# Optimization experiments

Hardware: AMD Instinct MI355X
Metric: run time of the kernel (lower is better)

The kernel has to match this reference:

```python
import jax, jax.numpy as jnp
import numpy as np
import math

D_MODEL = 1024
N_HEADS = 16
D_HEAD = D_MODEL // N_HEADS


def setup_inputs() -> dict:
    key = jax.random.key(0)
    ks = jax.random.split(key, 9)
    B, S = 4, 2048
    scale = 1.0 / math.sqrt(D_MODEL)
    x = jax.random.normal(ks[0], (B, S, D_MODEL), dtype=jnp.float32)
    # nn.Linear weights stored as [out, in]; we keep [in, out] for x @ W
    w_q = jax.random.uniform(ks[1], (D_MODEL, D_MODEL), jnp.float32, -scale, scale)
    b_q = jax.random.uniform(ks[2], (D_MODEL,), jnp.float32, -scale, scale)
    w_k = jax.random.uniform(ks[3], (D_MODEL, D_MODEL), jnp.float32, -scale, scale)
    b_k = jax.random.uniform(ks[4], (D_MODEL,), jnp.float32, -scale, scale)
    w_v = jax.random.uniform(ks[5], (D_MODEL, D_MODEL), jnp.float32, -scale, scale)
    b_v = jax.random.uniform(ks[6], (D_MODEL,), jnp.float32, -scale, scale)
    w_o = jax.random.uniform(ks[7], (D_MODEL, D_MODEL), jnp.float32, -scale, scale)
    b_o = jax.random.uniform(ks[8], (D_MODEL,), jnp.float32, -scale, scale)
    return {"x": x, "w_q": w_q, "b_q": b_q, "w_k": w_k, "b_k": b_k,
            "w_v": w_v, "b_v": b_v, "w_o": w_o, "b_o": b_o}


def reference(x, w_q, b_q, w_k, b_k, w_v, b_v, w_o, b_o):
    B, S, _ = x.shape
    def split_heads(t):  # [B,S,D] -> [B,H,S,Dh]
        return t.reshape(B, S, N_HEADS, D_HEAD).transpose(0, 2, 1, 3)
    q = split_heads(x @ w_q + b_q)
    k = split_heads(x @ w_k + b_k)
    v = split_heads(x @ w_v + b_v)
    scores = jnp.einsum('bhqd,bhkd->bhqk', q, k) / math.sqrt(D_HEAD)
    attn = jax.nn.softmax(scores, axis=-1)  # dropout p=0 -> identity
    ctx = jnp.einsum('bhqk,bhkd->bhqd', attn, v)
    ctx = ctx.transpose(0, 2, 1, 3).reshape(B, S, D_MODEL)
    return ctx @ w_o + b_o
```

## Files before the change

kernel.cpp:

```cpp
#include <hip/hip_runtime.h>
#include <hip/hip_bf16.h>

#define DM   1024
#define SEQ  2048
#define NH   16
#define DH   64
#define BH   64
#define MTOT 8192

typedef __attribute__((ext_vector_type(8)))  short short8;
typedef __attribute__((ext_vector_type(4)))  short short4v;
typedef __attribute__((ext_vector_type(4)))  float f32x4;
typedef __attribute__((ext_vector_type(16))) float f32x16;
typedef __attribute__((ext_vector_type(4)))  float fvec4;
typedef __attribute__((ext_vector_type(4)))  int   i32x4;
typedef unsigned short ushort_t;

#define AS1 __attribute__((address_space(1)))
#define AS3 __attribute__((address_space(3)))

#define QSCALE 0.18033688011112042f
#define THR_L2 11.541560327111707f

static __device__ __forceinline__ unsigned short f2bf(float f){
  __bf16 h = (__bf16)f;
  return __builtin_bit_cast(unsigned short, h);
}

static __device__ __forceinline__ float fexp2(float x){
  float r;
  asm("v_exp_f32 %0, %1\n\ts_nop 0" : "=v"(r) : "v"(x));
  return r;
}

static __device__ __forceinline__ void gld16(const void* g, void* l){
  __builtin_amdgcn_global_load_lds((const AS1 int*)g, (AS3 int*)l, 16, 0, 0);
}

__global__ void k_cast_x(const float* __restrict__ x, ushort_t* __restrict__ xb){
  const size_t i = (size_t)blockIdx.x*256 + threadIdx.x;
  const fvec4* xv = (const fvec4*)x;
  fvec4 a = xv[2*i], b = xv[2*i+1];
  short8 r;
  #pragma unroll
  for (int j=0;j<4;++j) r[j]   = (short)f2bf(a[j]);
  #pragma unroll
  for (int j=0;j<4;++j) r[4+j] = (short)f2bf(b[j]);
  ((short8*)xb)[i] = r;
}

__global__ void k_cast_wt(const float* __restrict__ wq, const float* __restrict__ wk,
                          const float* __restrict__ wv, const float* __restrict__ wo,
                          ushort_t* __restrict__ wt){
  const int z = blockIdx.y;
  const float* W = (z==0)?wq:(z==1)?wk:(z==2)?wv:wo;
  ushort_t* Wt = wt + (size_t)z*DM*DM;
  const int k0 = (blockIdx.x & 15)*64, n0 = (blockIdx.x >> 4)*64;
  __shared__ float tile[64][65];
  const int t = threadIdx.x;
  #pragma unroll
  for (int it=0; it<4; ++it){
    int c = it*256 + t;
    int rr = c>>4, cc = c&15;
    fvec4 v = *(const fvec4*)(W + (size_t)(k0+rr)*DM + n0 + cc*4);
    #pragma unroll
    for (int j=0;j<4;++j) tile[cc*4+j][rr] = v[j];
  }
  __syncthreads();
  #pragma unroll
  for (int it=0; it<4; ++it){
    int c = it*256 + t;
    int nn = c>>4, kk = c&15;
    short4v r;
    #pragma unroll
    for (int j=0;j<4;++j) r[j] = (short)f2bf(tile[nn][kk*4+j]);
    *(short4v*)(Wt + (size_t)(n0+nn)*DM + k0 + kk*4) = r;
  }
}

template<int MODE>
__global__ __launch_bounds__(256, 2)
void k_gemm128(const ushort_t* __restrict__ A, const ushort_t* __restrict__ WtBase,
               const float* __restrict__ b0, const float* __restrict__ b1,
               const float* __restrict__ b2,
               ushort_t* __restrict__ obf, float* __restrict__ of32){
  const int z = blockIdx.z;
  const ushort_t* Wt = WtBase + (size_t)z*DM*DM;
  const float* bias = (z==0)? b0 : (z==1? b1 : b2);
  __shared__ ushort_t Al[128*32];
  __shared__ ushort_t Bl[128*32];
  const int t = threadIdx.x;
  const int wid = t>>6, l = t&63, g = l>>4, li = l&15;
  const int m0 = blockIdx.x*128, n0 = blockIdx.y*128;
  const int wr = (wid>>1)*64, wc = (wid&1)*64;
  const int srow = t>>2, schunk = (t&3)*8;

  f32x4 acc[4][4] = {};

  for (int kt = 0; kt < DM; kt += 32){
    __syncthreads();
    #pragma unroll
    for (int c = 0; c < 2; ++c){
      gld16(A  + (size_t)(m0 + c*64 + srow)*DM + kt + schunk, (char*)Al + c*4096 + wid*1024);
      gld16(Wt + (size_t)(n0 + c*64 + srow)*DM + kt + schunk, (char*)Bl + c*4096 + wid*1024);
    }
    __syncthreads();
    short8 af[4], bw[4];
    #pragma unroll
    for (int mt=0; mt<4; ++mt)
      af[mt] = *(const short8*)(Al + (wr + mt*16 + li)*32 + g*8);
    #pragma unroll
    for (int nt=0; nt<4; ++nt)
      bw[nt] = *(const short8*)(Bl + (wc + nt*16 + li)*32 + g*8);
    #pragma unroll
    for (int mt=0; mt<4; ++mt)
      #pragma unroll
      for (int nt=0; nt<4; ++nt)
        acc[mt][nt] = __builtin_amdgcn_mfma_f32_16x16x32_bf16(af[mt], bw[nt], acc[mt][nt], 0,0,0);
  }

  if constexpr (MODE==0){
    if (z == 2){
      ushort_t* vt = obf + (size_t)2*MTOT*DM;
      #pragma unroll
      for (int nt=0; nt<4; ++nt){
        const int n = n0 + wc + nt*16 + li;
        const float bn = bias[n];
        const int h = n>>6, d = n&63;
        #pragma unroll
        for (int mt=0; mt<4; ++mt){
          const int m = m0 + wr + mt*16 + g*4;
          const int bb = m >> 11, s = m & 2047;
          short4v pk;
          #pragma unroll
          for (int r=0; r<4; ++r) pk[r] = (short)f2bf(acc[mt][nt][r] + bn);
          *(short4v*)(vt + (((size_t)(bb*NH + h)*DH + d)*SEQ + s)) = pk;
        }
      }
    } else {
      const float sc = (z==0) ? QSCALE : 1.f;
      #pragma unroll
      for (int nt=0; nt<4; ++nt){
        const int n = n0 + wc + nt*16 + li;
        const float bn = bias[n];
        #pragma unroll
        for (int mt=0; mt<4; ++mt){
          #pragma unroll
          for (int r=0; r<4; ++r){
            const int m = m0 + wr + mt*16 + g*4 + r;
            const float v = (acc[mt][nt][r] + bn)*sc;
            const int bb = m >> 11, s = m & 2047, h = n >> 6, d = n & 63;
            obf[(size_t)z*MTOT*DM + (((size_t)(bb*NH + h)*SEQ + s)*DH + d)] = f2bf(v);
          }
        }
      }
    }
  } else {
    #pragma unroll
    for (int nt=0; nt<4; ++nt){
      const int n = n0 + wc + nt*16 + li;
      const float bn = bias[n];
      #pragma unroll
      for (int mt=0; mt<4; ++mt){
        #pragma unroll
        for (int r=0; r<4; ++r){
          const int m = m0 + wr + mt*16 + g*4 + r;
          of32[(size_t)m*DM + n] = acc[mt][nt][r] + bn;
        }
      }
    }
  }
}

__global__ __launch_bounds__(256, 2)
void k_attn(const ushort_t* __restrict__ Qb, const ushort_t* __restrict__ Kb,
            const ushort_t* __restrict__ Vtb, ushort_t* __restrict__ ctx){
  const int bh = blockIdx.y, b = bh>>4, h = bh&15;
  const int t = threadIdx.x, wid = t>>6, lane = t&63;
  const int lq = lane&31, hi = lane>>5;
  const int qw = blockIdx.x*128 + wid*32;
  __shared__ ushort_t Kl[2][64*64];
  __shared__ ushort_t Vl[2][64*64];
  const ushort_t* Qh = Qb  + (size_t)bh*SEQ*DH;
  const ushort_t* Kh = Kb  + (size_t)bh*SEQ*DH;
  const ushort_t* Vh = Vtb + (size_t)bh*DH*SEQ;

  short8 qf[4];
  #pragma unroll
  for (int ks=0; ks<4; ++ks)
    qf[ks] = *(const short8*)(Qh + (size_t)(qw+lq)*DH + ks*16 + hi*8);

  f32x16 o0 = {}, o1 = {};
  float m_ = 0.f, ls = 0.f;

  const int srl = lane>>3, scp = lane&7;
  #define STAGE(kv0, bi) do {                                              \
    _Pragma("unroll")                                                      \
    for (int i8=0; i8<2; ++i8){                                            \
      const int row = wid*16 + i8*8 + srl;                                 \
      const int c = scp ^ (row&7);                                         \
      gld16(Kh + (size_t)((kv0)+row)*DH + c*8,                             \
            (char*)&Kl[bi][0] + (wid*16+i8*8)*128);                        \
      gld16(Vh + (size_t)row*SEQ + (kv0) + c*8,                            \
            (char*)&Vl[bi][0] + (wid*16+i8*8)*128);                        \
    }                                                                      \
  } while(0)

  STAGE(0, 0);
  __syncthreads();

  int cur = 0;
  for (int t64 = 0; t64 < SEQ/64; ++t64){
    if (t64 < SEQ/64 - 1){
      if (cur) STAGE((t64+1)*64, 0); else STAGE((t64+1)*64, 1);
    }
    const char* Kb_ = (const char*)&Kl[cur][0];
    const char* Vb_ = (const char*)&Vl[cur][0];

    short8 kf[8];
    #pragma unroll
    for (int blk=0; blk<2; ++blk){
      const int row = blk*32 + lq;
      #pragma unroll
      for (int ks=0; ks<4; ++ks)
        kf[blk*4+ks] = *(const short8*)(Kb_ + row*128 + (((2*ks+hi) ^ (row&7))<<4));
    }
    f32x16 s0 = {}, s1 = {};
    __builtin_amdgcn_s_setprio(1);
    #pragma unroll
    for (int ks=0; ks<4; ++ks){
      s0 = __builtin_amdgcn_mfma_f32_32x32x16_bf16(kf[ks],   qf[ks], s0, 0,0,0);
      s1 = __builtin_amdgcn_mfma_f32_32x32x16_bf16(kf[4+ks], qf[ks], s1, 0,0,0);
    }
    __builtin_amdgcn_s_setprio(0);

    float tm = s0[0];
    #pragma unroll
    for (int r=1; r<16; ++r) tm = fmaxf(tm, s0[r]);
    #pragma unroll
    for (int r=0; r<16; ++r) tm = fmaxf(tm, s1[r]);
    tm = fmaxf(tm, __shfl_xor(tm, 32));

    if (!__all(tm <= m_ + THR_L2)){
      const float mn = fmaxf(m_, tm);
      const float fac = fexp2(m_ - mn);
      m_ = mn; ls *= fac;
      #pragma unroll
      for (int r=0; r<16; ++r){
        const float fr = __shfl(fac, (r&3) + 8*(r>>2) + 4*hi);
        o0[r] *= fr; o1[r] *= fr;
      }
    }
    #pragma unroll
    for (int r=0; r<16; ++r){ float e = fexp2(s0[r]-m_); s0[r]=e; ls+=e; }
    #pragma unroll
    for (int r=0; r<16; ++r){ float e = fexp2(s1[r]-m_); s1[r]=e; ls+=e; }

    short8 pa[4];
    #pragma unroll
    for (int blk=0; blk<2; ++blk){
      #pragma unroll
      for (int half=0; half<2; ++half){
        i32x4 w;
        #pragma unroll
        for (int wp=0; wp<2; ++wp){
          const int base = half*8 + 2*wp;
          float a0 = blk ? s1[base]   : s0[base];
          float a1 = blk ? s1[base+1] : s0[base+1];
          float c0 = blk ? s1[base+4] : s0[base+4];
          float c1 = blk ? s1[base+5] : s0[base+5];
          int x, y;
          asm("v_cvt_pk_bf16_f32 %0, %1, %2" : "=v"(x) : "v"(a0), "v"(a1));
          asm("v_cvt_pk_bf16_f32 %0, %1, %2" : "=v"(y) : "v"(c0), "v"(c1));
          asm("v_permlane32_swap_b32 %0, %1" : "+v"(x), "+v"(y));
          w[wp] = x; w[2+wp] = y;
        }
        pa[blk*2+half] = __builtin_bit_cast(short8, w);
      }
    }

    short8 vb[8];
    #pragma unroll
    for (int dblk=0; dblk<2; ++dblk){
      const int row = dblk*32 + lq;
      #pragma unroll
      for (int ks=0; ks<4; ++ks)
        vb[dblk*4+ks] = *(const short8*)(Vb_ + row*128 + (((2*ks+hi) ^ (row&7))<<4));
    }
    __builtin_amdgcn_s_setprio(1);
    #pragma unroll
    for (int ks=0; ks<4; ++ks){
      o0 = __builtin_amdgcn_mfma_f32_32x32x16_bf16(pa[ks], vb[ks],   o0, 0,0,0);
      o1 = __builtin_amdgcn_mfma_f32_32x32x16_bf16(pa[ks], vb[4+ks], o1, 0,0,0);
    }
    __builtin_amdgcn_s_setprio(0);

    __syncthreads();
    cur ^= 1;
  }

  ls += __shfl_xor(ls, 32);
  const float inv = 1.f / ls;
  #pragma unroll
  for (int r=0; r<16; ++r){
    const float ir = __shfl(inv, (r&3) + 8*(r>>2) + 4*hi);
    const int qrow = qw + (r&3) + 8*(r>>2) + 4*hi;
    ushort_t* dst = ctx + ((size_t)(b*SEQ + qrow))*DM + h*DH;
    dst[lq]    = f2bf(o0[r]*ir);
    dst[32+lq] = f2bf(o1[r]*ir);
  }
  #undef STAGE
}

extern "C" void kernel_launch(void* const* d_in, const int* in_sizes, int n_in,
                              void* d_out, int out_size, void* d_ws, size_t ws_size,
                              hipStream_t stream){
  const float* x  = (const float*)d_in[0];
  const float* wq = (const float*)d_in[1];
  const float* bq = (const float*)d_in[2];
  const float* wk = (const float*)d_in[3];
  const float* bk = (const float*)d_in[4];
  const float* wv = (const float*)d_in[5];
  const float* bv = (const float*)d_in[6];
  const float* wo = (const float*)d_in[7];
  const float* bo = (const float*)d_in[8];
  float* out = (float*)d_out;

  ushort_t* xb  = (ushort_t*)d_ws;
  ushort_t* wt  = xb  + (size_t)MTOT*DM;
  ushort_t* qkv = wt  + (size_t)4*DM*DM;
  ushort_t* ctx = qkv + (size_t)3*MTOT*DM;

  k_cast_x<<<4096, 256, 0, stream>>>(x, xb);
  k_cast_wt<<<dim3(256,4), 256, 0, stream>>>(wq, wk, wv, wo, wt);
  k_gemm128<0><<<dim3(64,8,3), 256, 0, stream>>>(xb, wt, bq, bk, bv, qkv, nullptr);
  k_attn<<<dim3(16,64), 256, 0, stream>>>(qkv, qkv + (size_t)MTOT*DM, qkv + (size_t)2*MTOT*DM, ctx);
  k_gemm128<1><<<dim3(64,8,1), 256, 0, stream>>>(ctx, wt + (size_t)3*DM*DM, bo, bo, bo, nullptr, out);
}
```

Measured before the change: 284.0 us.

## Compute softmax row sums via MFMA with ones and restructure LDS layout

The row-sum accumulation moves from per-element VALU adds into an extra MFMA that multiplies the bf16 probabilities by a ones vector, so the sum is taken over the same bf16-rounded values used for P·V. The row max reduction now uses v_max3 to cut VALU instruction count. The K/V LDS staging layout changes from an XOR-swizzled row layout to a column-chunk-major layout, so each lane reads at a simple strided offset without swizzle arithmetic. The extra MFMA adds matrix-core work per tile, and the new layout may introduce LDS bank conflicts.

Result: slower. 290.1 us (+2.2%).

```diff
diff --git a/kernel.cpp b/kernel.cpp
--- a/kernel.cpp
+++ b/kernel.cpp
@@ -31,6 +31,12 @@
   float r;
   asm("v_exp_f32 %0, %1\n\ts_nop 0" : "=v"(r) : "v"(x));
   return r;
+}
+
+static __device__ __forceinline__ float fmax3(float a, float b, float c){
+  float d;
+  asm("v_max3_f32 %0, %1, %2, %3" : "=v"(d) : "v"(a), "v"(b), "v"(c));
+  return d;
 }
 
 static __device__ __forceinline__ void gld16(const void* g, void* l){
@@ -179,8 +185,8 @@
   const int t = threadIdx.x, wid = t>>6, lane = t&63;
   const int lq = lane&31, hi = lane>>5;
   const int qw = blockIdx.x*128 + wid*32;
-  __shared__ ushort_t Kl[2][64*64];
-  __shared__ ushort_t Vl[2][64*64];
+  __shared__ ushort_t Kl[2][4096];
+  __shared__ ushort_t Vl[2][4096];
   const ushort_t* Qh = Qb  + (size_t)bh*SEQ*DH;
   const ushort_t* Kh = Kb  + (size_t)bh*SEQ*DH;
   const ushort_t* Vh = Vtb + (size_t)bh*DH*SEQ;
@@ -190,19 +196,19 @@
   for (int ks=0; ks<4; ++ks)
     qf[ks] = *(const short8*)(Qh + (size_t)(qw+lq)*DH + ks*16 + hi*8);
 
-  f32x16 o0 = {}, o1 = {};
-  float m_ = 0.f, ls = 0.f;
-
-  const int srl = lane>>3, scp = lane&7;
+  short8 ones8;
+  #pragma unroll
+  for (int j=0;j<8;++j) ones8[j] = (short)0x3F80;
+
+  f32x16 o0 = {}, o1 = {}, lsa = {};
+  float m_ = 0.f;
+
   #define STAGE(kv0, bi) do {                                              \
     _Pragma("unroll")                                                      \
-    for (int i8=0; i8<2; ++i8){                                            \
-      const int row = wid*16 + i8*8 + srl;                                 \
-      const int c = scp ^ (row&7);                                         \
-      gld16(Kh + (size_t)((kv0)+row)*DH + c*8,                             \
-            (char*)&Kl[bi][0] + (wid*16+i8*8)*128);                        \
-      gld16(Vh + (size_t)row*SEQ + (kv0) + c*8,                            \
-            (char*)&Vl[bi][0] + (wid*16+i8*8)*128);                        \
+    for (int i=0; i<2; ++i){                                               \
+      const int c = wid*2 + i;                                             \
+      gld16(Kh + (size_t)((kv0)+lane)*DH + c*8, (char*)&Kl[bi][0] + c*1024);\
+      gld16(Vh + (size_t)lane*SEQ + (kv0) + c*8, (char*)&Vl[bi][0] + c*1024);\
     }                                                                      \
   } while(0)
 
@@ -214,16 +220,14 @@
     if (t64 < SEQ/64 - 1){
       if (cur) STAGE((t64+1)*64, 0); else STAGE((t64+1)*64, 1);
     }
-    const char* Kb_ = (const char*)&Kl[cur][0];
-    const char* Vb_ = (const char*)&Vl[cur][0];
+    const char* Kb_ = (const char*)&Kl[cur][0] + hi*1024 + lq*16;
+    const char* Vb_ = (const char*)&Vl[cur][0] + hi*1024 + lq*16;
 
     short8 kf[8];
     #pragma unroll
-    for (int blk=0; blk<2; ++blk){
-      const int row = blk*32 + lq;
-      #pragma unroll
-      for (int ks=0; ks<4; ++ks)
-        kf[blk*4+ks] = *(const short8*)(Kb_ + row*128 + (((2*ks+hi) ^ (row&7))<<4));
+    for (int ks=0; ks<4; ++ks){
+      kf[ks]   = *(const short8*)(Kb_ + ks*2048);
+      kf[4+ks] = *(const short8*)(Kb_ + ks*2048 + 512);
     }
     f32x16 s0 = {}, s1 = {};
     __builtin_amdgcn_s_setprio(1);
@@ -234,27 +238,32 @@
     }
     __builtin_amdgcn_s_setprio(0);
 
-    float tm = s0[0];
-    #pragma unroll
-    for (int r=1; r<16; ++r) tm = fmaxf(tm, s0[r]);
-    #pragma unroll
-    for (int r=0; r<16; ++r) tm = fmaxf(tm, s1[r]);
+    float mx[8];
+    #pragma unroll
+    for (int i=0;i<8;++i) mx[i] = fmax3(s0[i], s0[8+i], s1[i]);
+    float y0 = fmax3(mx[0], mx[4], s1[8]);
+    float y1 = fmax3(mx[1], mx[5], s1[9]);
+    float y2 = fmax3(mx[2], mx[6], s1[10]);
+    float y3 = fmax3(mx[3], mx[7], s1[11]);
+    float z0 = fmax3(y0, y1, s1[12]);
+    float z1 = fmax3(y2, y3, s1[13]);
+    float tm = fmax3(fmax3(z0, z1, s1[14]), s1[15], -1e30f);
     tm = fmaxf(tm, __shfl_xor(tm, 32));
 
     if (!__all(tm <= m_ + THR_L2)){
       const float mn = fmaxf(m_, tm);
       const float fac = fexp2(m_ - mn);
-      m_ = mn; ls *= fac;
+      m_ = mn;
       #pragma unroll
       for (int r=0; r<16; ++r){
         const float fr = __shfl(fac, (r&3) + 8*(r>>2) + 4*hi);
-        o0[r] *= fr; o1[r] *= fr;
-      }
-    }
-    #pragma unroll
-    for (int r=0; r<16; ++r){ float e = fexp2(s0[r]-m_); s0[r]=e; ls+=e; }
-    #pragma unroll
-    for (int r=0; r<16; ++r){ float e = fexp2(s1[r]-m_); s1[r]=e; ls+=e; }
+        o0[r] *= fr; o1[r] *= fr; lsa[r] *= fr;
+      }
+    }
+    #pragma unroll
+    for (int r=0; r<16; ++r) s0[r] = fexp2(s0[r]-m_);
+    #pragma unroll
+    for (int r=0; r<16; ++r) s1[r] = fexp2(s1[r]-m_);
 
     short8 pa[4];
     #pragma unroll
@@ -281,17 +290,16 @@
 
     short8 vb[8];
     #pragma unroll
-    for (int dblk=0; dblk<2; ++dblk){
-      const int row = dblk*32 + lq;
-      #pragma unroll
-      for (int ks=0; ks<4; ++ks)
-        vb[dblk*4+ks] = *(const short8*)(Vb_ + row*128 + (((2*ks+hi) ^ (row&7))<<4));
+    for (int ks=0; ks<4; ++ks){
+      vb[ks]   = *(const short8*)(Vb_ + ks*2048);
+      vb[4+ks] = *(const short8*)(Vb_ + ks*2048 + 512);
     }
     __builtin_amdgcn_s_setprio(1);
     #pragma unroll
     for (int ks=0; ks<4; ++ks){
-      o0 = __builtin_amdgcn_mfma_f32_32x32x16_bf16(pa[ks], vb[ks],   o0, 0,0,0);
-      o1 = __builtin_amdgcn_mfma_f32_32x32x16_bf16(pa[ks], vb[4+ks], o1, 0,0,0);
+      o0  = __builtin_amdgcn_mfma_f32_32x32x16_bf16(pa[ks], vb[ks],   o0, 0,0,0);
+      o1  = __builtin_amdgcn_mfma_f32_32x32x16_bf16(pa[ks], vb[4+ks], o1, 0,0,0);
+      lsa = __builtin_amdgcn_mfma_f32_32x32x16_bf16(pa[ks], ones8,    lsa, 0,0,0);
     }
     __builtin_amdgcn_s_setprio(0);
 
@@ -299,15 +307,13 @@
     cur ^= 1;
   }
 
-  ls += __shfl_xor(ls, 32);
-  const float inv = 1.f / ls;
   #pragma unroll
   for (int r=0; r<16; ++r){
-    const float ir = __shfl(inv, (r&3) + 8*(r>>2) + 4*hi);
+    const float iv = 1.f / lsa[r];
     const int qrow = qw + (r&3) + 8*(r>>2) + 4*hi;
     ushort_t* dst = ctx + ((size_t)(b*SEQ + qrow))*DM + h*DH;
-    dst[lq]    = f2bf(o0[r]*ir);
-    dst[32+lq] = f2bf(o1[r]*ir);
+    dst[lq]    = f2bf(o0[r]*iv);
+    dst[32+lq] = f2bf(o1[r]*iv);
   }
   #undef STAGE
 }
```
